# Optimization experiments

Measured on AMD Instinct MI355X. Metric: run time of the kernel, lower is better.

Reference implementation:

```python
import jax, jax.numpy as jnp
import numpy as np

B = 1024       # batch of triples
E = 50000      # num_entities
R = 500        # num_relations
D = 512        # dimension
P = 16         # parts
C = 8          # num_cores
ALPHA = 2.0    # -> q = alpha/2 = 1.0
Q = ALPHA / 2.0
DP = D // P    # 32


def setup_inputs() -> dict:
    key = jax.random.key(0)
    ks = jax.random.split(key, 10)
    xav_e = (2.0 / (E + D)) ** 0.5
    xav_r = (2.0 / (R + D)) ** 0.5
    return {
        "heads": jax.random.randint(ks[0], (B,), 0, E),
        "relations": jax.random.randint(ks[1], (B,), 0, R),
        "tails": jax.random.randint(ks[2], (B,), 0, E),
        "entity_w": jax.random.normal(ks[3], (E, D), dtype=jnp.float32) * xav_e,
        "relation_w": jax.random.normal(ks[4], (R, D), dtype=jnp.float32) * xav_r,
        "W_cores": jax.random.uniform(ks[5], (C, P, P, P), dtype=jnp.float32,
                                      minval=-0.01, maxval=0.01),
        "attn_w1": jax.random.normal(ks[6], (2 * D, D), dtype=jnp.float32) * (1.0 / (2 * D)) ** 0.5,
        "attn_b1": jnp.zeros((D,), dtype=jnp.float32),
        "attn_w2": jax.random.normal(ks[7], (D, C), dtype=jnp.float32) * (1.0 / D) ** 0.5,
        "attn_b2": jnp.zeros((C,), dtype=jnp.float32),
    }


def _pq_norm(x):
    # ((|x|^p).sum(2) ** q).sum(1), p=2
    return ((x * x).sum(2) ** Q).sum(1)


def _geometric_consistency(W_cores):
    # center of mass of |W| along each axis, per core; vectorized over cores
    coords = jnp.arange(P, dtype=jnp.float32)
    Wa = jnp.abs(W_cores)                      # [C,P,P,P]
    tot = Wa.sum(axis=(1, 2, 3))               # [C]
    cx = (Wa * coords[None, :, None, None]).sum(axis=(1, 2, 3)) / tot
    cy = (Wa * coords[None, None, :, None]).sum(axis=(1, 2, 3)) / tot
    cz = (Wa * coords[None, None, None, :]).sum(axis=(1, 2, 3)) / tot
    centers = jnp.stack([cx, cy, cz], axis=1)  # [C,3]
    d2 = ((centers[:, None, :] - centers[None, :, :]) ** 2).sum(-1)
    dist = jnp.sqrt(d2)
    masked = dist + jnp.eye(C, dtype=dist.dtype) * 1e6
    min_d = masked.min(axis=1)
    return -jnp.mean(jnp.log(min_d + 1e-6))


def reference(heads, relations, tails, entity_w, relation_w, W_cores,
              attn_w1, attn_b1, attn_w2, attn_b2):
    h = entity_w[heads]          # [B,D]
    r = relation_w[relations]    # [B,D]
    t = entity_w[tails]          # [B,D]

    hr = jnp.concatenate([h, r], axis=1)                       # [B,2D]
    hid = jax.nn.relu(hr @ attn_w1 + attn_b1)                  # [B,D]
    attn = jax.nn.softmax(hid @ attn_w2 + attn_b2, axis=1)     # [B,C]

    h3 = h.reshape(-1, DP, P)
    r3 = r.reshape(-1, DP, P)
    t3 = t.reshape(-1, DP, P)

    h_norm = _pq_norm(h3)
    r_norm = _pq_norm(r3)
    t_norm = _pq_norm(t3)

    # attention-weighted effective core per triple (sum over cores is linear,
    # so folding attn into W before the contraction is exactly the same math)
    Weff = jnp.einsum('bc,cpqs->bpqs', attn, W_cores)          # [B,P,P,P]

    # x1[b,i,s] = sum_{p,q} h[b,i,p] r[b,i,q] W[b,p,q,s]
    x1 = jnp.einsum('bip,biq,bpqs->bis', h3, r3, Weff)
    # x2[b,i,p] = sum_{q,s} r[b,i,q] t[b,i,s] W[b,p,q,s]
    x2 = jnp.einsum('biq,bis,bpqs->bip', r3, t3, Weff)
    # x3[b,i,q] = sum_{p,s} h[b,i,p] t[b,i,s] W[b,p,q,s]
    x3 = jnp.einsum('bip,bis,bpqs->biq', h3, t3, Weff)

    whr_norm = _pq_norm(x1)
    wrt_norm = _pq_norm(x2)
    wth_norm = _pq_norm(x3)

    scores = x1.reshape(-1, D) @ entity_w.T                    # [B,E]

    factor1 = jnp.mean(h_norm) + jnp.mean(r_norm) + jnp.mean(t_norm)
    factor2 = jnp.mean(whr_norm) + jnp.mean(wrt_norm) + jnp.mean(wth_norm)
    factor3 = _geometric_consistency(W_cores)
    return (scores, factor1, factor2, factor3, attn)
```

## Files before the change

### kernel.cpp

```cpp
#include <hip/hip_runtime.h>
#include <cstdint>
#include <cstddef>

#define NB 1024
#define NE 50000
#define NE_PAD 50048
#define DCOL 512
#define ATTN_C 8

static const size_t SCORES_OFF = (size_t)NB * NE;
static const size_t F1_OFF = SCORES_OFF + 0;
static const size_t F2_OFF = SCORES_OFF + 1;
static const size_t F3_OFF = SCORES_OFF + 2;
static const size_t ATTN_OFF = SCORES_OFF + 3;

typedef float f32x4 __attribute__((ext_vector_type(4)));
typedef short s16x8 __attribute__((ext_vector_type(8)));

__device__ __forceinline__ unsigned short f2bf(float f) {
  union { float f; uint32_t u; } x; x.f = f;
  uint32_t u = x.u;
  uint32_t r = (u + 0x7fffu + ((u >> 16) & 1u)) >> 16;
  return (unsigned short)r;
}

__device__ __forceinline__ void gload16(const void* g, void* l) {
  __builtin_amdgcn_global_load_lds(
      (const __attribute__((address_space(1))) uint32_t*)g,
      (__attribute__((address_space(3))) uint32_t*)l, 16, 0, 0);
}

template <int N>
__device__ __forceinline__ void waitcnt_vm() {
  static_assert(N == 0 || N == 4 || N == 8, "literal dispatch");
  if constexpr (N == 0) asm volatile("s_waitcnt vmcnt(0)" ::: "memory");
  else if constexpr (N == 4) asm volatile("s_waitcnt vmcnt(4)" ::: "memory");
  else if constexpr (N == 8) asm volatile("s_waitcnt vmcnt(8)" ::: "memory");
}

__global__ __launch_bounds__(256)
void prep(const int* __restrict__ heads, const int* __restrict__ rels,
          const int* __restrict__ tails, const float* __restrict__ ew,
          const float* __restrict__ rw, const float* __restrict__ w1,
          unsigned short* __restrict__ hrb, unsigned short* __restrict__ w1t,
          unsigned short* __restrict__ ewb, float* __restrict__ n1) {
  int tid = threadIdx.x;
  if (blockIdx.x < NB) {
    int b = blockIdx.x;
    const float* h = ew + (size_t)heads[b] * DCOL;
    const float* r = rw + (size_t)rels[b] * DCOL;
    const float* t = ew + (size_t)tails[b] * DCOL;
    float acc = 0.f;
    #pragma unroll
    for (int it = 0; it < 2; ++it) {
      int d = it * 256 + tid;
      float hv = h[d], rv = r[d], tv = t[d];
      hrb[(size_t)b * 1024 + d] = f2bf(hv);
      hrb[(size_t)b * 1024 + DCOL + d] = f2bf(rv);
      acc += hv * hv + rv * rv + tv * tv;
    }
    __shared__ float red[256];
    red[tid] = acc; __syncthreads();
    for (int s = 128; s > 0; s >>= 1) {
      if (tid < s) red[tid] += red[tid + s];
      __syncthreads();
    }
    if (tid == 0) n1[b] = red[0];
  } else if (blockIdx.x < NB + 512) {
    int tb = blockIdx.x - NB;
    int nb = (tb & 15) * 32, kb = (tb >> 4) * 32;
    __shared__ float tile[32][33];
    int tx = tid & 31, ty = tid >> 5;
    #pragma unroll
    for (int rr = 0; rr < 32; rr += 8)
      tile[ty + rr][tx] = w1[(size_t)(kb + ty + rr) * 512 + nb + tx];
    __syncthreads();
    #pragma unroll
    for (int rr = 0; rr < 32; rr += 8)
      w1t[(size_t)(nb + ty + rr) * 1024 + kb + tx] = f2bf(tile[tx][ty + rr]);
  } else {
    const int n4valid = NE * DCOL / 4;
    const int n4tot = NE_PAD * DCOL / 4;
    int i = (blockIdx.x - NB - 512) * 256 + tid;
    const int stride = 2048 * 256;
    for (; i < n4tot; i += stride) {
      float x = 0.f, y = 0.f, z = 0.f, w = 0.f;
      if (i < n4valid) {
        float4 v = ((const float4*)ew)[i];
        x = v.x; y = v.y; z = v.z; w = v.w;
      }
      union { unsigned short u[4]; uint2 v2; } o;
      o.u[0] = f2bf(x); o.u[1] = f2bf(y); o.u[2] = f2bf(z); o.u[3] = f2bf(w);
      ((uint2*)ewb)[i] = o.v2;
    }
  }
}

template <int EPI, int FR, int MT, int KTOT>
__global__ __launch_bounds__(256, 2)
void gemm_nt(const unsigned short* __restrict__ A,
             const unsigned short* __restrict__ B,
             float* __restrict__ C, const float* __restrict__ bias,
             int Nc, int total_tiles, int nblocks) {
  constexpr int BM = FR * 32;
  constexpr int TILE = BM * 128;
  constexpr int NKT = KTOT / 64;
  constexpr int SOPS = 2 * FR;
  __shared__ __align__(16) uint8_t smem[4 * TILE];
  const int tid = threadIdx.x;
  const int lane = tid & 63;
  const int wv = tid >> 6;
  const int wm = wv >> 1, wn = wv & 1;
  constexpr int RBY = KTOT * 2;

  const int per_xcd = total_tiles >> 3;
  const int xcd = blockIdx.x & 7;
  const int lstride = nblocks >> 3;
  int l = blockIdx.x >> 3;
  if (l >= per_xcd) return;

  f32x4 acc[FR][FR];
  #pragma unroll
  for (int i = 0; i < FR; ++i)
    #pragma unroll
    for (int j = 0; j < FR; ++j) acc[i][j] = (f32x4){0.f, 0.f, 0.f, 0.f};

  const int srow = lane >> 3;
  const int scol = lane & 7;

  auto stage = [&](int kt, int buf, int m0, int n0) {
    #pragma unroll
    for (int j = 0; j < FR; ++j) {
      const int chunk = wv * FR + j;
      const int r = chunk * 8 + srow;
      const int c = scol ^ (r & 7);
      gload16((const uint8_t*)A + (size_t)(m0 + r) * RBY + kt * 128 + c * 16,
              &smem[buf * 2 * TILE + chunk * 1024]);
      gload16((const uint8_t*)B + (size_t)(n0 + r) * RBY + kt * 128 + c * 16,
              &smem[buf * 2 * TILE + TILE + chunk * 1024]);
    }
  };
  auto compute = [&](int buf) {
    const uint8_t* sa = &smem[buf * 2 * TILE];
    const uint8_t* sb = sa + TILE;
    #pragma unroll
    for (int kk = 0; kk < 2; ++kk) {
      s16x8 af[FR], bfv[FR];
      #pragma unroll
      for (int f = 0; f < FR; ++f) {
        const int ra = wm * 16 * FR + f * 16 + (lane & 15);
        const int ca = (kk * 4 + (lane >> 4)) ^ (ra & 7);
        af[f] = *(const s16x8*)&sa[ra * 128 + ca * 16];
        const int rb = wn * 16 * FR + f * 16 + (lane & 15);
        const int cb = (kk * 4 + (lane >> 4)) ^ (rb & 7);
        bfv[f] = *(const s16x8*)&sb[rb * 128 + cb * 16];
      }
      #pragma unroll
      for (int fm = 0; fm < FR; ++fm)
        #pragma unroll
        for (int fn = 0; fn < FR; ++fn)
          acc[fm][fn] = __builtin_amdgcn_mfma_f32_16x16x32_bf16(
              af[fm], bfv[fn], acc[fm][fn], 0, 0, 0);
    }
  };

  int w = xcd * per_xcd + l;
  int m0 = (w % MT) * BM, n0 = (w / MT) * BM;
  stage(0, 0, m0, n0);
  stage(1, 1, m0, n0);

  const int rl = lane >> 4, cl = lane & 15;
  while (true) {
    const int ln = l + lstride;
    const bool lastt = ln >= per_xcd;
    int m0n = m0, n0n = n0;
    if (!lastt) {
      int wn2 = xcd * per_xcd + ln;
      m0n = (wn2 % MT) * BM; n0n = (wn2 / MT) * BM;
    }
    #pragma unroll
    for (int k = 0; k < NKT; ++k) {
      const int c = k & 1;
      if (lastt && k == NKT - 1) waitcnt_vm<0>();
      else waitcnt_vm<SOPS>();
      __builtin_amdgcn_sched_barrier(0);
      __builtin_amdgcn_s_barrier();
      __builtin_amdgcn_sched_barrier(0);
      compute(c);
      __builtin_amdgcn_sched_barrier(0);
      __builtin_amdgcn_s_barrier();
      __builtin_amdgcn_sched_barrier(0);
      if (k + 2 < NKT) stage(k + 2, c, m0, n0);
      else if (!lastt) stage(k + 2 - NKT, c, m0n, n0n);
      __builtin_amdgcn_sched_barrier(0);
    }
    #pragma unroll
    for (int fm = 0; fm < FR; ++fm)
      #pragma unroll
      for (int fn = 0; fn < FR; ++fn)
        #pragma unroll
        for (int j = 0; j < 4; ++j) {
          int gm = m0 + wm * 16 * FR + fm * 16 + rl * 4 + j;
          int gn = n0 + wn * 16 * FR + fn * 16 + cl;
          if (gn < Nc) {
            float v = acc[fm][fn][j];
            if (EPI) v = fmaxf(v + bias[gn], 0.f);
            C[(size_t)gm * Nc + gn] = v;
          }
          acc[fm][fn][j] = 0.f;
        }
    if (lastt) break;
    l = ln; m0 = m0n; n0 = n0n;
  }
}

__global__ __launch_bounds__(256, 2)
void triple_core(const int* __restrict__ heads, const int* __restrict__ rels,
                 const int* __restrict__ tails, const float* __restrict__ ew,
                 const float* __restrict__ rw, const float* __restrict__ wc,
                 const float* __restrict__ hid, const float* __restrict__ w2,
                 const float* __restrict__ b2, float* __restrict__ attn_out,
                 unsigned short* __restrict__ x1b, float* __restrict__ n2) {
  __shared__ float hs[512], rs[512], ts[512];
  __shared__ __align__(16) float W123[4096][4];
  __shared__ float att[8];
  __shared__ float wred[4][8];
  __shared__ float red[256];
  int b = blockIdx.x, tid = threadIdx.x;
  int lane = tid & 63, wid = tid >> 6;
  const float* hp_ = ew + (size_t)heads[b] * DCOL;
  const float* rp_ = rw + (size_t)rels[b] * DCOL;
  const float* tp_ = ew + (size_t)tails[b] * DCOL;
  float la[8] = {0, 0, 0, 0, 0, 0, 0, 0};
  #pragma unroll
  for (int it = 0; it < 2; ++it) {
    int d = it * 256 + tid;
    hs[d] = hp_[d]; rs[d] = rp_[d]; ts[d] = tp_[d];
    float hv = hid[(size_t)b * DCOL + d];
    #pragma unroll
    for (int c = 0; c < 8; ++c) la[c] = fmaf(hv, w2[d * 8 + c], la[c]);
  }
  #pragma unroll
  for (int off = 32; off > 0; off >>= 1)
    #pragma unroll
    for (int c = 0; c < 8; ++c) la[c] += __shfl_down(la[c], off);
  if (lane == 0)
    #pragma unroll
    for (int c = 0; c < 8; ++c) wred[wid][c] = la[c];
  __syncthreads();
  if (tid == 0) {
    float lg[8];
    #pragma unroll
    for (int c = 0; c < 8; ++c)
      lg[c] = wred[0][c] + wred[1][c] + wred[2][c] + wred[3][c] + b2[c];
    float mx = lg[0];
    #pragma unroll
    for (int c = 1; c < 8; ++c) mx = fmaxf(mx, lg[c]);
    float e[8], s = 0.f;
    #pragma unroll
    for (int c = 0; c < 8; ++c) { e[c] = expf(lg[c] - mx); s += e[c]; }
    #pragma unroll
    for (int c = 0; c < 8; ++c) {
      float a = e[c] / s;
      att[c] = a;
      attn_out[(size_t)b * 8 + c] = a;
    }
  }
  __syncthreads();
  #pragma unroll
  for (int it = 0; it < 16; ++it) {
    int idx = it * 256 + tid;
    float w = 0.f;
    #pragma unroll
    for (int c = 0; c < 8; ++c) w = fmaf(att[c], wc[c * 4096 + idx], w);
    int s = idx & 15, q = (idx >> 4) & 15, p = idx >> 8;
    W123[idx][0] = w;
    W123[(q * 16 + s) * 16 + p][1] = w;
    W123[(p * 16 + s) * 16 + q][2] = w;
  }
  __syncthreads();

  const int so = tid & 15;
  const int i0 = tid >> 4, i1 = i0 + 16;
  float h0[16], r0[16], t0[16], h1[16], r1[16], t1[16];
  #pragma unroll
  for (int k = 0; k < 16; ++k) {
    h0[k] = hs[i0 * 16 + k]; r0[k] = rs[i0 * 16 + k]; t0[k] = ts[i0 * 16 + k];
    h1[k] = hs[i1 * 16 + k]; r1[k] = rs[i1 * 16 + k]; t1[k] = ts[i1 * 16 + k];
  }
  float a10 = 0.f, a20 = 0.f, a30 = 0.f, a11 = 0.f, a21 = 0.f, a31 = 0.f;
  const float4* wp = (const float4*)&W123[so][0];
  #pragma unroll
  for (int u = 0; u < 16; ++u) {
    #pragma unroll
    for (int v = 0; v < 16; ++v) {
      float4 w = wp[u * 256 + v * 16];
      a10 = fmaf(h0[u] * r0[v], w.x, a10);
      a20 = fmaf(r0[u] * t0[v], w.y, a20);
      a30 = fmaf(h0[u] * t0[v], w.z, a30);
      a11 = fmaf(h1[u] * r1[v], w.x, a11);
      a21 = fmaf(r1[u] * t1[v], w.y, a21);
      a31 = fmaf(h1[u] * t1[v], w.z, a31);
    }
  }
  x1b[(size_t)b * 512 + i0 * 16 + so] = f2bf(a10);
  x1b[(size_t)b * 512 + i1 * 16 + so] = f2bf(a11);
  red[tid] = a10 * a10 + a20 * a20 + a30 * a30
           + a11 * a11 + a21 * a21 + a31 * a31;
  __syncthreads();
  for (int s = 128; s > 0; s >>= 1) {
    if (tid < s) red[tid] += red[tid + s];
    __syncthreads();
  }
  if (tid == 0) n2[b] = red[0];
}

__global__ __launch_bounds__(256)
void finalize(const float* __restrict__ n1, const float* __restrict__ n2,
              const float* __restrict__ wc, float* __restrict__ out) {
  int tid = threadIdx.x;
  __shared__ float red[256];
  float a = 0.f;
  for (int i = tid; i < NB; i += 256) a += n1[i];
  red[tid] = a; __syncthreads();
  for (int s = 128; s > 0; s >>= 1) { if (tid < s) red[tid] += red[tid + s]; __syncthreads(); }
  if (tid == 0) out[F1_OFF] = red[0] / (float)NB;
  __syncthreads();
  a = 0.f;
  for (int i = tid; i < NB; i += 256) a += n2[i];
  red[tid] = a; __syncthreads();
  for (int s = 128; s > 0; s >>= 1) { if (tid < s) red[tid] += red[tid + s]; __syncthreads(); }
  if (tid == 0) out[F2_OFF] = red[0] / (float)NB;
  __syncthreads();

  int c = tid >> 5, l = tid & 31;
  float tot = 0.f, cx = 0.f, cy = 0.f, cz = 0.f;
  for (int e = l; e < 4096; e += 32) {
    float w = fabsf(wc[c * 4096 + e]);
    int z = e & 15, y = (e >> 4) & 15, x = e >> 8;
    tot += w; cx += w * x; cy += w * y; cz += w * z;
  }
  #pragma unroll
  for (int off = 16; off > 0; off >>= 1) {
    tot += __shfl_down(tot, off);
    cx += __shfl_down(cx, off);
    cy += __shfl_down(cy, off);
    cz += __shfl_down(cz, off);
  }
  __shared__ float cent[8][3];
  if (l == 0) { cent[c][0] = cx / tot; cent[c][1] = cy / tot; cent[c][2] = cz / tot; }
  __syncthreads();
  if (tid == 0) {
    float f3 = 0.f;
    for (int i = 0; i < 8; ++i) {
      float mn = 1e30f;
      for (int j = 0; j < 8; ++j) {
        if (j == i) continue;
        float dx = cent[i][0] - cent[j][0];
        float dy = cent[i][1] - cent[j][1];
        float dz = cent[i][2] - cent[j][2];
        float d = sqrtf(dx * dx + dy * dy + dz * dz);
        mn = fminf(mn, d);
      }
      f3 += logf(mn + 1e-6f);
    }
    out[F3_OFF] = -f3 / 8.f;
  }
}

extern "C" void kernel_launch(void* const* d_in, const int* in_sizes, int n_in,
                              void* d_out, int out_size, void* d_ws, size_t ws_size,
                              hipStream_t stream) {
  const int* heads = (const int*)d_in[0];
  const int* rels = (const int*)d_in[1];
  const int* tails = (const int*)d_in[2];
  const float* ew = (const float*)d_in[3];
  const float* rw = (const float*)d_in[4];
  const float* wc = (const float*)d_in[5];
  const float* w1 = (const float*)d_in[6];
  const float* b1 = (const float*)d_in[7];
  const float* w2 = (const float*)d_in[8];
  const float* b2 = (const float*)d_in[9];
  float* out = (float*)d_out;

  uint8_t* ws = (uint8_t*)d_ws;
  const size_t EWB_SZ = (size_t)NE_PAD * DCOL * 2;
  unsigned short* ewb = (unsigned short*)ws;
  unsigned short* hrb = (unsigned short*)(ws + EWB_SZ);
  unsigned short* w1t = (unsigned short*)(ws + EWB_SZ + 2097152);
  float* hid = (float*)(ws + EWB_SZ + 2097152 + 1048576);
  unsigned short* x1b = (unsigned short*)(ws + EWB_SZ + 2097152 + 1048576 + 2097152);
  float* n1 = (float*)(ws + EWB_SZ + 2097152 + 1048576 + 2097152 + 1048576);
  float* n2 = n1 + NB;

  prep<<<NB + 512 + 2048, 256, 0, stream>>>(heads, rels, tails, ew, rw, w1,
                                            hrb, w1t, ewb, n1);
  gemm_nt<1, 2, 16, 1024><<<128, 256, 0, stream>>>(
      hrb, w1t, hid, b1, 512, 128, 128);
  triple_core<<<NB, 256, 0, stream>>>(heads, rels, tails, ew, rw, wc,
                                      hid, w2, b2, out + ATTN_OFF, x1b, n2);
  gemm_nt<0, 4, 8, 512><<<512, 256, 0, stream>>>(
      x1b, ewb, out, nullptr, NE, 3128, 512);
  finalize<<<1, 256, 0, stream>>>(n1, n2, wc, out);
}
```

Before: 217.8 us.

## Defer GEMM tile epilogue stores to overlap with next tile's main loop

For the FR=4 persistent GEMM path, accumulators of a finished tile are copied to a second register set and written to global memory in slices interleaved with the next tile's K-loop iterations. The vmcnt waits are adjusted (8/16/24) to account for the extra outstanding stores. This aims to hide the epilogue store latency behind MFMA work, at the cost of doubling accumulator registers, which may add pressure or spills.

```diff
diff --git a/kernel.cpp b/kernel.cpp
--- a/kernel.cpp
+++ b/kernel.cpp
@@ -32,10 +32,12 @@
 
 template <int N>
 __device__ __forceinline__ void waitcnt_vm() {
-  static_assert(N == 0 || N == 4 || N == 8, "literal dispatch");
+  static_assert(N == 0 || N == 4 || N == 8 || N == 16 || N == 24, "literal");
   if constexpr (N == 0) asm volatile("s_waitcnt vmcnt(0)" ::: "memory");
   else if constexpr (N == 4) asm volatile("s_waitcnt vmcnt(4)" ::: "memory");
   else if constexpr (N == 8) asm volatile("s_waitcnt vmcnt(8)" ::: "memory");
+  else if constexpr (N == 16) asm volatile("s_waitcnt vmcnt(16)" ::: "memory");
+  else if constexpr (N == 24) asm volatile("s_waitcnt vmcnt(24)" ::: "memory");
 }
 
 __global__ __launch_bounds__(256)
@@ -119,7 +121,7 @@
   int l = blockIdx.x >> 3;
   if (l >= per_xcd) return;
 
-  f32x4 acc[FR][FR];
+  f32x4 acc[FR][FR], acc2[FR][FR];
   #pragma unroll
   for (int i = 0; i < FR; ++i)
     #pragma unroll
@@ -127,6 +129,7 @@
 
   const int srow = lane >> 3;
   const int scol = lane & 7;
+  const int rl = lane >> 4, cl = lane & 15;
 
   auto stage = [&](int kt, int buf, int m0, int n0) {
     #pragma unroll
@@ -163,37 +166,7 @@
               af[fm], bfv[fn], acc[fm][fn], 0, 0, 0);
     }
   };
-
-  int w = xcd * per_xcd + l;
-  int m0 = (w % MT) * BM, n0 = (w / MT) * BM;
-  stage(0, 0, m0, n0);
-  stage(1, 1, m0, n0);
-
-  const int rl = lane >> 4, cl = lane & 15;
-  while (true) {
-    const int ln = l + lstride;
-    const bool lastt = ln >= per_xcd;
-    int m0n = m0, n0n = n0;
-    if (!lastt) {
-      int wn2 = xcd * per_xcd + ln;
-      m0n = (wn2 % MT) * BM; n0n = (wn2 / MT) * BM;
-    }
-    #pragma unroll
-    for (int k = 0; k < NKT; ++k) {
-      const int c = k & 1;
-      if (lastt && k == NKT - 1) waitcnt_vm<0>();
-      else waitcnt_vm<SOPS>();
-      __builtin_amdgcn_sched_barrier(0);
-      __builtin_amdgcn_s_barrier();
-      __builtin_amdgcn_sched_barrier(0);
-      compute(c);
-      __builtin_amdgcn_sched_barrier(0);
-      __builtin_amdgcn_s_barrier();
-      __builtin_amdgcn_sched_barrier(0);
-      if (k + 2 < NKT) stage(k + 2, c, m0, n0);
-      else if (!lastt) stage(k + 2 - NKT, c, m0n, n0n);
-      __builtin_amdgcn_sched_barrier(0);
-    }
+  auto store_direct = [&](int m0, int n0) {
     #pragma unroll
     for (int fm = 0; fm < FR; ++fm)
       #pragma unroll
@@ -209,7 +182,83 @@
           }
           acc[fm][fn][j] = 0.f;
         }
-    if (lastt) break;
+  };
+
+  int w = xcd * per_xcd + l;
+  int m0 = (w % MT) * BM, n0 = (w / MT) * BM;
+  int m0p = 0, n0p = 0;
+  int deep = 0;
+  stage(0, 0, m0, n0);
+  stage(1, 1, m0, n0);
+
+  while (true) {
+    const int ln = l + lstride;
+    const bool lastt = ln >= per_xcd;
+    int m0n = m0, n0n = n0;
+    if (!lastt) {
+      int w2 = xcd * per_xcd + ln;
+      m0n = (w2 % MT) * BM; n0n = (w2 / MT) * BM;
+    }
+    #pragma unroll
+    for (int k = 0; k < NKT; ++k) {
+      const int c = k & 1;
+      if (lastt && k == NKT - 1) {
+        waitcnt_vm<0>();
+      } else if constexpr (FR == 4) {
+        if (deep == 0) waitcnt_vm<8>();
+        else if (deep == 1) {
+          if (k == 0) waitcnt_vm<8>();
+          else if (k == 1) waitcnt_vm<16>();
+          else waitcnt_vm<24>();
+        } else waitcnt_vm<24>();
+      } else {
+        waitcnt_vm<SOPS>();
+      }
+      __builtin_amdgcn_sched_barrier(0);
+      __builtin_amdgcn_s_barrier();
+      __builtin_amdgcn_sched_barrier(0);
+      compute(c);
+      __builtin_amdgcn_sched_barrier(0);
+      __builtin_amdgcn_s_barrier();
+      __builtin_amdgcn_sched_barrier(0);
+      if (k + 2 < NKT) stage(k + 2, c, m0, n0);
+      else if (!lastt) stage(k + 2 - NKT, c, m0n, n0n);
+      __builtin_amdgcn_sched_barrier(0);
+      if constexpr (FR == 4) {
+        if (deep > 0) {
+          const int fm = k >> 1;
+          #pragma unroll
+          for (int fi = 0; fi < 2; ++fi) {
+            const int fn = (k & 1) * 2 + fi;
+            #pragma unroll
+            for (int j = 0; j < 4; ++j) {
+              const int gm = m0p + wm * 64 + fm * 16 + rl * 4 + j;
+              const int gn = n0p + wn * 64 + fn * 16 + cl;
+              C[(size_t)gm * Nc + gn] = acc2[fm][fn][j];
+            }
+          }
+          __builtin_amdgcn_sched_barrier(0);
+        }
+      }
+    }
+    if (lastt) {
+      store_direct(m0, n0);
+      break;
+    }
+    if (FR == 4 && (n0 + BM) <= Nc) {
+      #pragma unroll
+      for (int fm = 0; fm < FR; ++fm)
+        #pragma unroll
+        for (int fn = 0; fn < FR; ++fn) {
+          acc2[fm][fn] = acc[fm][fn];
+          acc[fm][fn] = (f32x4){0.f, 0.f, 0.f, 0.f};
+        }
+      m0p = m0; n0p = n0;
+      deep = (deep > 0) ? 2 : 1;
+    } else {
+      store_direct(m0, n0);
+      deep = 0;
+    }
     l = ln; m0 = m0n; n0 = n0n;
   }
 }
```

Result: slower. 229.0 us (+5.1%).
